# Kernel tuning notes

Hardware: AMD Instinct MI355X
Metric: run time of the kernel (lower is better)

Reference implementation:

```python
import jax, jax.numpy as jnp
import numpy as np
import math

B, D, L, H, K, CONV_N = 32, 128, 1024, 8, 7, 4
DK = D // H
EPS = 1e-5


def make_pos_encoding():
    i = np.arange(D, dtype=np.float64)
    freqs = np.where(i % 2 == 0, 10000.0 ** (-i / D), -(10000.0 ** ((1 - i) / D)))
    phases = np.where(i % 2 == 0, 0.0, math.pi / 2)
    pos = np.arange(L, dtype=np.float64)[None, :]  # [1, L]
    pe = np.sin(pos * freqs[:, None] + phases[:, None])  # [D, L]
    return jnp.asarray(pe, dtype=jnp.float32)


def layer_norm_2d(x, w, b):
    # nn.LayerNorm([D, L]) on [B, D, L]: normalize jointly over last two dims
    mu = jnp.mean(x, axis=(1, 2), keepdims=True)
    var = jnp.var(x, axis=(1, 2), keepdims=True)
    return (x - mu) * jax.lax.rsqrt(var + EPS) * w[None] + b[None]


def setup_inputs():
    key = jax.random.key(0)
    ks = jax.random.split(key, 24)
    s = 0.05
    x = jax.random.normal(ks[0], (B, D, L), jnp.float32)
    lengths = jax.random.randint(ks[1], (B,), L // 2, L + 1)
    mask = (jnp.arange(L)[None, :] >= lengths[:, None]).astype(jnp.float32)  # 1 = pad
    inp = {
        "x": x,
        "mask": mask,
        "pos_enc": make_pos_encoding(),
        "normb_w": jnp.ones((D, L), jnp.float32),
        "normb_b": jnp.zeros((D, L), jnp.float32),
        "dw_w": jax.random.normal(ks[2], (CONV_N, D, K), jnp.float32) * s,
        "dw_b": jnp.zeros((CONV_N, D), jnp.float32),
        "pw_w": jax.random.normal(ks[3], (CONV_N, D, D), jnp.float32) * s,
        "pw_b": jnp.zeros((CONV_N, D), jnp.float32),
        "norms_w": jnp.ones((CONV_N, D, L), jnp.float32),
        "norms_b": jnp.zeros((CONV_N, D, L), jnp.float32),
        "qw": jax.random.normal(ks[4], (D, D), jnp.float32) * s,
        "qb": jnp.zeros((D,), jnp.float32),
        "kw": jax.random.normal(ks[5], (D, D), jnp.float32) * s,
        "kb": jnp.zeros((D,), jnp.float32),
        "vw": jax.random.normal(ks[6], (D, D), jnp.float32) * s,
        "vb": jnp.zeros((D,), jnp.float32),
        "aw": jax.random.normal(ks[7], (D, D), jnp.float32) * s,  # attention output fc
        "ab": jnp.zeros((D,), jnp.float32),
        "norme_w": jnp.ones((D, L), jnp.float32),
        "norme_b": jnp.zeros((D, L), jnp.float32),
        "fw": jax.random.normal(ks[8], (D, D), jnp.float32) * s,  # final fc
        "fb": jnp.zeros((D,), jnp.float32),
    }
    return inp


def reference(x, mask, pos_enc, normb_w, normb_b, dw_w, dw_b, pw_w, pw_b,
              norms_w, norms_b, qw, qb, kw, kb, vw, vb, aw, ab,
              norme_w, norme_b, fw, fb):
    # positional encoding + pre-LN
    out = x + pos_enc[None]
    res = out
    out = layer_norm_2d(out, normb_w, normb_b)

    # conv stack (eval mode: dropout is identity)
    for i in range(CONV_N):
        h = jax.lax.conv_general_dilated(
            out, dw_w[i][:, None, :],  # depthwise: [D, 1, K]
            window_strides=(1,), padding=[(K // 2, K // 2)],
            dimension_numbers=("NCH", "OIH", "NCH"),
            feature_group_count=D) + dw_b[i][None, :, None]
        h = jnp.einsum("bcl,oc->bol", h, pw_w[i]) + pw_b[i][None, :, None]
        out = jax.nn.relu(h) + res
        res = out
        out = layer_norm_2d(out, norms_w[i], norms_b[i])

    # multi-head self-attention (manual bmm-softmax-bmm, scale 1/sqrt(d_k))
    xt = jnp.swapaxes(out, 1, 2)  # [B, L, D]
    q = (xt @ qw.T + qb).reshape(B, L, H, DK)
    k = (xt @ kw.T + kb).reshape(B, L, H, DK)
    v = (xt @ vw.T + vb).reshape(B, L, H, DK)
    scores = jnp.einsum("bqhd,bkhd->bhqk", q, k) * (1.0 / math.sqrt(DK))
    m = mask[:, None, None, :]  # broadcast over heads and query dim
    scores = scores * (1.0 - m) + m * (-1e30)
    attn = jax.nn.softmax(scores, axis=-1)
    o = jnp.einsum("bhqk,bkhd->bqhd", attn, v).reshape(B, L, D)
    o = o @ aw.T + ab
    o = jnp.swapaxes(o, 1, 2)  # [B, D, L]

    out = o + res
    res = out
    out = layer_norm_2d(out, norme_w, norme_b)
    out = jnp.einsum("bdl,ed->bel", out, fw) + fb[None, :, None]
    out = jax.nn.relu(out) + res
    return out
```

## Files before the change

### kernel.cpp

```cpp
#include <hip/hip_runtime.h>

#define NB 32
#define ND 128
#define NL 1024
#define NDL (ND*NL)
#define STATS_B 16
#define STATS_R (32*STATS_B)

typedef __attribute__((ext_vector_type(8))) short bf16x8;
typedef __attribute__((ext_vector_type(4))) float f32x4;

__device__ __forceinline__ f32x4 mfma_bf16_16x16x32(bf16x8 a, bf16x8 b, f32x4 c) {
#if defined(__HIP_DEVICE_COMPILE__)
  return __builtin_amdgcn_mfma_f32_16x16x32_bf16(a, b, c, 0, 0, 0);
#else
  return c;
#endif
}

__device__ __forceinline__ float exp2fast(float x) {
#if defined(__HIP_DEVICE_COMPILE__) && __has_builtin(__builtin_amdgcn_exp2f)
  return __builtin_amdgcn_exp2f(x);
#elif defined(__HIP_DEVICE_COMPILE__)
  return __expf(x * 0.6931471805599453f);
#else
  return x;
#endif
}

__device__ __forceinline__ unsigned short bf16rnd(float f) {
  union { float f; unsigned u; } c; c.f = f;
  return (unsigned short)((c.u + 0x7FFFu + ((c.u >> 16) & 1u)) >> 16);
}
__device__ __forceinline__ unsigned packpair(float a, float b) {
  return (unsigned)bf16rnd(a) | ((unsigned)bf16rnd(b) << 16);
}
__device__ __forceinline__ unsigned packtrunc(float a, float b) {
  unsigned ua = __float_as_uint(a), ub = __float_as_uint(b);
  return (ub & 0xFFFF0000u) | (ua >> 16);
}
__device__ __forceinline__ bf16x8 packbf8(float4 a, float4 b) {
  union { unsigned u[4]; bf16x8 v; } r;
  r.u[0] = packpair(a.x, a.y); r.u[1] = packpair(a.z, a.w);
  r.u[2] = packpair(b.x, b.y); r.u[3] = packpair(b.z, b.w);
  return r.v;
}

__device__ __forceinline__ void blockRedAtomic(float s, float sq, float* base) {
  __shared__ float red[16];
#pragma unroll
  for (int off = 32; off > 0; off >>= 1) {
    s  += __shfl_down(s, off, 64);
    sq += __shfl_down(sq, off, 64);
  }
  int wave = threadIdx.x >> 6;
  int nw = blockDim.x >> 6;
  if ((threadIdx.x & 63) == 0) { red[wave*2] = s; red[wave*2+1] = sq; }
  __syncthreads();
  if (threadIdx.x == 0) {
    float ts = 0.f, tq = 0.f;
    for (int i = 0; i < nw; ++i) { ts += red[i*2]; tq += red[i*2+1]; }
    unsafeAtomicAdd(base,     ts);
    unsafeAtomicAdd(base + 1, tq);
  }
}

__global__ void k_zero(float* stats) {
  int t = threadIdx.x;
#pragma unroll
  for (int i = 0; i < 3; ++i) stats[i*1024 + t] = 0.f;
}

__global__ __launch_bounds__(256) void k_addpos(const float* __restrict__ x,
                                                const float* __restrict__ pe,
                                                float* __restrict__ res,
                                                float* __restrict__ stats0) {
  int b = blockIdx.x >> 6;
  int off = ((blockIdx.x & 63) << 11) + (threadIdx.x << 3);
  const float4* xp = (const float4*)(x + (size_t)b*NDL + off);
  const float4* pp = (const float4*)(pe + off);
  float4* rp = (float4*)(res + (size_t)b*NDL + off);
  float s = 0.f, sq = 0.f;
#pragma unroll
  for (int i = 0; i < 2; ++i) {
    float4 a = xp[i], p = pp[i];
    float4 r;
    r.x = a.x + p.x; r.y = a.y + p.y; r.z = a.z + p.z; r.w = a.w + p.w;
    rp[i] = r;
    s  += r.x + r.y + r.z + r.w;
    sq += r.x*r.x + r.y*r.y + r.z*r.z + r.w*r.w;
  }
  blockRedAtomic(s, sq, stats0 + b*STATS_B);
}


__device__ __forceinline__ void load_w_frags16(const float* __restrict__ W,
                                               int wo, int lo, int hi, bf16x8 af[4]) {
#pragma unroll
  for (int kk = 0; kk < 4; ++kk) {
    const float4* wp = (const float4*)(W + (size_t)(wo + lo)*128 + kk*32 + hi*8);
    af[kk] = packbf8(wp[0], wp[1]);
  }
}

__device__ __forceinline__ void mfma_core16(const unsigned* xs, bf16x8 af[4],
                                            int lo, int hi, f32x4 acc[4]) {
#pragma unroll
  for (int ln = 0; ln < 4; ++ln) {
#pragma unroll
    for (int kk = 0; kk < 4; ++kk) {
      int l = ln*16 + lo;
      int off = (l*256 + kk*64 + hi*16) ^ ((lo & 7) << 4);
      bf16x8 bf = *(const bf16x8*)((const char*)xs + off);
      acc[ln] = mfma_bf16_16x16x32(af[kk], bf, acc[ln]);
    }
  }
}

__device__ __forceinline__ void conv_row(const float* __restrict__ srow,
                                         const float* __restrict__ lwrow,
                                         const float* __restrict__ lbrow,
                                         int base, float mu, float rstd,
                                         const float* wk, float bias0,
                                         float* h ) {
  float wa[14];
  bool interior = (base >= 4) && (base + 12 <= NL);
  if (interior) {
    const float4* sp = (const float4*)(srow + base - 4);
    const float4* wp = (const float4*)(lwrow + base - 4);
    const float4* bp = (const float4*)(lbrow + base - 4);
#pragma unroll
    for (int qd = 0; qd < 4; ++qd) {
      float4 s4 = sp[qd], w4 = wp[qd], b4 = bp[qd];
      float sv[4] = {s4.x, s4.y, s4.z, s4.w};
      float wv[4] = {w4.x, w4.y, w4.z, w4.w};
      float bv[4] = {b4.x, b4.y, b4.z, b4.w};
#pragma unroll
      for (int e = 0; e < 4; ++e) {
        int j = qd*4 + e - 1;
        if (j >= 0 && j < 14)
          wa[j] = (sv[e] - mu)*rstd*wv[e] + bv[e];
      }
    }
  } else {
#pragma unroll
    for (int j = 0; j < 14; ++j) {
      int gl = base + j - 3;
      float v = 0.f;
      if (gl >= 0 && gl < NL)
        v = (srow[gl] - mu)*rstd*lwrow[gl] + lbrow[gl];
      wa[j] = v;
    }
  }
#pragma unroll
  for (int l = 0; l < 8; ++l) {
    float acc = bias0;
#pragma unroll
    for (int j = 0; j < 7; ++j) acc += wa[l+j]*wk[j];
    h[l] = acc;
  }
}

template<int MODE>
__global__ __launch_bounds__(512) void k_gemm_mfma(
    const float* __restrict__ src, const unsigned short* __restrict__ srcb16,
    const float* __restrict__ W, const float* __restrict__ bias,
    const float* __restrict__ resbuf, float* __restrict__ wrbuf,
    const float* __restrict__ lnw, const float* __restrict__ lnb,
    const float* __restrict__ dww, const float* __restrict__ dwb,
    const float* __restrict__ statsIn, float* __restrict__ statsOut) {
  __shared__ unsigned xs[4096];
  int b  = blockIdx.x >> 4;
  int l0 = (blockIdx.x & 15) << 6;
  int tid = threadIdx.x;
  int wave = tid >> 6, lane = tid & 63;
  int lo = lane & 15, hi = lane >> 4;
  int wo = wave * 16;

  float mu = 0.f, rstd = 0.f;
  if (MODE == 0 || MODE == 3) {
    mu = statsIn[b*STATS_B] * (1.f/NDL);
    rstd = rsqrtf(statsIn[b*STATS_B + 1]*(1.f/NDL) - mu*mu + 1e-5f);
  }

  if (MODE == 0) {
    int c2 = tid >> 3, lq = tid & 7;
    int c = c2*2, base = l0 + lq*8;
    float wk0[7], wk1[7];
#pragma unroll
    for (int j = 0; j < 7; ++j) { wk0[j] = dww[c*7 + j]; wk1[j] = dww[(c+1)*7 + j]; }
    const float* sa  = src + (size_t)b*NDL + (size_t)c*NL;
    const float* la  = lnw + (size_t)c*NL;
    const float* lbv = lnb + (size_t)c*NL;
    float h0[8], h1[8];
    conv_row(sa,      la,      lbv,      base, mu, rstd, wk0, dwb[c],   h0);
    conv_row(sa + NL, la + NL, lbv + NL, base, mu, rstd, wk1, dwb[c+1], h1);
#pragma unroll
    for (int l = 0; l < 8; ++l) {
      int ll = lq*8 + l;
      xs[(ll << 6) | (c2 ^ ((ll & 7) << 2))] = packpair(h0[l], h1[l]);
    }
  } else if (MODE == 1) {
    for (int i = tid; i < 1024; i += 512) {
      int c2 = i >> 4, lq = (i & 15) << 2;
      int c = c2*2;
      const unsigned short* sp = srcb16 + (size_t)b*NDL + (size_t)c*NL + l0 + lq;
      uint2 ra = *(const uint2*)sp;
      uint2 rb = *(const uint2*)(sp + NL);
      unsigned wv[4];
      wv[0] = (ra.x & 0xFFFFu) | (rb.x << 16);
      wv[1] = (ra.x >> 16)     | (rb.x & 0xFFFF0000u);
      wv[2] = (ra.y & 0xFFFFu) | (rb.y << 16);
      wv[3] = (ra.y >> 16)     | (rb.y & 0xFFFF0000u);
#pragma unroll
      for (int j = 0; j < 4; ++j) {
        int l = lq + j;
        xs[(l << 6) | (c2 ^ ((l & 7) << 2))] = wv[j];
      }
    }
  } else {
    for (int i = tid; i < 1024; i += 512) {
      int c2 = i >> 4, lq = (i & 15) << 2;
      int c = c2*2;
      const float* sp = src + (size_t)b*NDL + (size_t)c*NL + l0 + lq;
      float4 v0 = *(const float4*)sp;
      float4 v1 = *(const float4*)(sp + NL);
      size_t gi = (size_t)c*NL + l0 + lq;
      float4 w0 = *(const float4*)(lnw + gi), w1 = *(const float4*)(lnw + gi + NL);
      float4 bb0 = *(const float4*)(lnb + gi), bb1 = *(const float4*)(lnb + gi + NL);
      float va[4] = {(v0.x-mu)*rstd*w0.x + bb0.x, (v0.y-mu)*rstd*w0.y + bb0.y,
                     (v0.z-mu)*rstd*w0.z + bb0.z, (v0.w-mu)*rstd*w0.w + bb0.w};
      float vb[4] = {(v1.x-mu)*rstd*w1.x + bb1.x, (v1.y-mu)*rstd*w1.y + bb1.y,
                     (v1.z-mu)*rstd*w1.z + bb1.z, (v1.w-mu)*rstd*w1.w + bb1.w};
#pragma unroll
      for (int j = 0; j < 4; ++j) {
        int l = lq + j;
        xs[(l << 6) | (c2 ^ ((l & 7) << 2))] = packpair(va[j], vb[j]);
      }
    }
  }

  bf16x8 af[4];
  load_w_frags16(W, wo, lo, hi, af);
  f32x4 acc[4];
#pragma unroll
  for (int ln = 0; ln < 4; ++ln) acc[ln] = (f32x4){0.f,0.f,0.f,0.f};

  __syncthreads();
  mfma_core16(xs, af, lo, hi, acc);

  if (MODE == 0 || MODE == 1) {
    float s = 0.f, sq = 0.f;
#pragma unroll
    for (int ln = 0; ln < 4; ++ln) {
      int l = l0 + ln*16 + lo;
#pragma unroll
      for (int r = 0; r < 4; ++r) {
        int o = wo + hi*4 + r;
        size_t gi = ((size_t)b*ND + o)*NL + l;
        float v = acc[ln][r] + bias[o];
        if (MODE == 0) v = fmaxf(v, 0.f);
        v += resbuf[gi];
        wrbuf[gi] = v;
        s += v; sq += v*v;
      }
    }
    blockRedAtomic(s, sq, statsOut + b*STATS_B);
  } else {
#pragma unroll
    for (int ln = 0; ln < 4; ++ln) {
      int l = l0 + ln*16 + lo;
#pragma unroll
      for (int r = 0; r < 4; ++r) {
        int o = wo + hi*4 + r;
        size_t gi = ((size_t)b*ND + o)*NL + l;
        wrbuf[gi] = fmaxf(acc[ln][r] + bias[o], 0.f) + resbuf[gi];
      }
    }
  }
}

__global__ __launch_bounds__(512) void k_qkv_mfma(
    const float* __restrict__ src,
    const float* __restrict__ qw, const float* __restrict__ kw, const float* __restrict__ vw,
    const float* __restrict__ qb, const float* __restrict__ kb, const float* __restrict__ vb,
    unsigned short* __restrict__ qo, unsigned short* __restrict__ ko,
    unsigned short* __restrict__ vo,
    const float* __restrict__ lnw, const float* __restrict__ lnb,
    const float* __restrict__ statsIn) {
  __shared__ unsigned xs[4096];
  int b  = blockIdx.x >> 4;
  int l0 = (blockIdx.x & 15) << 6;
  int tid = threadIdx.x;
  int wave = tid >> 6, lane = tid & 63;
  int lo = lane & 15, hi = lane >> 4;
  int wo = wave * 16;

  float mu = statsIn[b*STATS_B] * (1.f/NDL);
  float rstd = rsqrtf(statsIn[b*STATS_B + 1]*(1.f/NDL) - mu*mu + 1e-5f);
  for (int i = tid; i < 1024; i += 512) {
    int c2 = i >> 4, lq = (i & 15) << 2;
    int c = c2*2;
    const float* sp = src + (size_t)b*NDL + (size_t)c*NL + l0 + lq;
    float4 v0 = *(const float4*)sp;
    float4 v1 = *(const float4*)(sp + NL);
    size_t gi = (size_t)c*NL + l0 + lq;
    float4 w0 = *(const float4*)(lnw + gi), w1 = *(const float4*)(lnw + gi + NL);
    float4 bb0 = *(const float4*)(lnb + gi), bb1 = *(const float4*)(lnb + gi + NL);
    float va[4] = {(v0.x-mu)*rstd*w0.x + bb0.x, (v0.y-mu)*rstd*w0.y + bb0.y,
                   (v0.z-mu)*rstd*w0.z + bb0.z, (v0.w-mu)*rstd*w0.w + bb0.w};
    float vb[4] = {(v1.x-mu)*rstd*w1.x + bb1.x, (v1.y-mu)*rstd*w1.y + bb1.y,
                   (v1.z-mu)*rstd*w1.z + bb1.z, (v1.w-mu)*rstd*w1.w + bb1.w};
#pragma unroll
    for (int j = 0; j < 4; ++j) {
      int l = lq + j;
      xs[(l << 6) | (c2 ^ ((l & 7) << 2))] = packpair(va[j], vb[j]);
    }
  }
  __syncthreads();

  const float* Ws[3] = {qw, kw, vw};
  const float* Bs[3] = {qb, kb, vb};
  unsigned short* Os[3] = {qo, ko, vo};
#pragma unroll 1
  for (int mat = 0; mat < 3; ++mat) {
    bf16x8 af[4];
    load_w_frags16(Ws[mat], wo, lo, hi, af);
    f32x4 acc[4];
#pragma unroll
    for (int ln = 0; ln < 4; ++ln) acc[ln] = (f32x4){0.f,0.f,0.f,0.f};
    mfma_core16(xs, af, lo, hi, acc);
    float oscale = (mat == 0) ? 0.25f*1.4426950408889634f : 1.0f;
    const float* bias = Bs[mat];
    unsigned short* op = Os[mat];
#pragma unroll
    for (int ln = 0; ln < 4; ++ln) {
      int l = l0 + ln*16 + lo;
      int o4 = wo + hi*4;
      float vx = (acc[ln][0] + bias[o4+0]) * oscale;
      float vy = (acc[ln][1] + bias[o4+1]) * oscale;
      float vz = (acc[ln][2] + bias[o4+2]) * oscale;
      float vw4 = (acc[ln][3] + bias[o4+3]) * oscale;
      uint2 pk; pk.x = packpair(vx, vy); pk.y = packpair(vz, vw4);
      *(uint2*)(op + ((size_t)b*NL + l)*ND + o4) = pk;
    }
  }
}

template<bool MASKED>
__device__ __forceinline__ void attn_tile(bf16x8 kf0, bf16x8 kf1, bf16x8 vf,
                                          const bf16x8 qf[4], f32x4 acc[4],
                                          float denp[4], int kb, int len, int hi) {
#pragma unroll
  for (int qt = 0; qt < 4; ++qt) {
    f32x4 z = (f32x4){0.f,0.f,0.f,0.f};
    f32x4 s0 = mfma_bf16_16x16x32(kf0, qf[qt], z);
    f32x4 s1 = mfma_bf16_16x16x32(kf1, qf[qt], z);
    float e[8];
#pragma unroll
    for (int r = 0; r < 4; ++r) {
      float e0 = exp2fast(s0[r]);
      float e1 = exp2fast(s1[r]);
      if (MASKED) {
        e0 = (kb + hi*4 + r < len)      ? e0 : 0.f;
        e1 = (kb + 16 + hi*4 + r < len) ? e1 : 0.f;
      }
      e[r] = e0; e[r+4] = e1;
    }
    denp[qt] += ((e[0]+e[1])+(e[2]+e[3])) + ((e[4]+e[5])+(e[6]+e[7]));
    union { unsigned u[4]; bf16x8 v; } pu;
    pu.u[0] = packtrunc(e[0], e[1]);
    pu.u[1] = packtrunc(e[2], e[3]);
    pu.u[2] = packtrunc(e[4], e[5]);
    pu.u[3] = packtrunc(e[6], e[7]);
    acc[qt] = mfma_bf16_16x16x32(vf, pu.v, acc[qt]);
  }
}

__global__ __launch_bounds__(512) void k_attn_fused(
    const unsigned short* __restrict__ q, const unsigned short* __restrict__ k,
    const unsigned short* __restrict__ v, const float* __restrict__ mask,
    unsigned short* __restrict__ att_t) {
  __shared__ short kv[32768];
  __shared__ int slen_sh;
  int bid = blockIdx.x;
  int b  = bid >> 4;
  int h  = (bid >> 1) & 7;
  int qh = bid & 1;
  int tid = threadIdx.x;
  const float* mrow = mask + (size_t)b*NL;

  if (tid == 0) slen_sh = 0;
  __syncthreads();
  {
    int cnt = 0;
    for (int i = tid; i < NL; i += 512) cnt += (mrow[i] == 0.f) ? 1 : 0;
#pragma unroll
    for (int off = 32; off > 0; off >>= 1) cnt += __shfl_down(cnt, off, 64);
    if ((tid & 63) == 0) atomicAdd(&slen_sh, cnt);
  }
  __syncthreads();
  int len = slen_sh;
  int nkt = (len + 31) >> 5;
  int kstage = nkt << 5;

  for (int idx = tid; idx < 4096; idx += 512) {
    int key = idx >> 2, dq = idx & 3;
    if (key >= kstage) break;
    int dk = dq*4;
    uint2 kd; kd.x = 0u; kd.y = 0u;
    if (key < len) kd = *(const uint2*)(k + ((size_t)b*NL + key)*ND + h*16 + dk);
    int kt = key >> 5, w = key & 31;
    int t16 = w >> 4, klo = w & 15;
    int khi = dk >> 3, ii = dk & 7;
    unsigned* dst = (unsigned*)(kv + kt*512 + t16*256 + (khi*16 + klo)*8 + ii);
    dst[0] = kd.x; dst[1] = kd.y;
  }
  for (int idx = tid; idx < 2048; idx += 512) {
    int keyp = idx >> 2, vq = idx & 3;
    int key = keyp*2;
    if (key >= kstage) break;
    int vlo = vq*4;
    uint2 ra, rb; ra.x = ra.y = rb.x = rb.y = 0u;
    size_t voff = ((size_t)b*NL + key)*ND + h*16 + vlo;
    if (key < len)     ra = *(const uint2*)(v + voff);
    if (key + 1 < len) rb = *(const uint2*)(v + voff + ND);
    unsigned wv[4];
    wv[0] = (ra.x & 0xFFFFu) | (rb.x << 16);
    wv[1] = (ra.x >> 16)     | (rb.x & 0xFFFF0000u);
    wv[2] = (ra.y & 0xFFFFu) | (rb.y << 16);
    wv[3] = (ra.y >> 16)     | (rb.y & 0xFFFF0000u);
    int kt = key >> 5, w = key & 31;
    int vhi, ii;
    if (w < 16) { vhi = w >> 2; ii = w & 3; }
    else        { vhi = (w - 16) >> 2; ii = 4 + (w & 3); }
#pragma unroll
    for (int e = 0; e < 4; ++e)
      *(unsigned*)(kv + 16384 + kt*512 + (vhi*16 + vlo + e)*8 + ii) = wv[e];
  }
  __syncthreads();

  int wave = tid >> 6, lane = tid & 63;
  int lo = lane & 15, hi = lane >> 4;
  int q0 = qh*512 + wave*64;

  bf16x8 qf[4];
#pragma unroll
  for (int qt = 0; qt < 4; ++qt) {
    if (hi < 2) {
      union { uint4 u; bf16x8 v; } qu;
      qu.u = *(const uint4*)(q + ((size_t)b*NL + q0 + qt*16 + lo)*ND + h*16 + hi*8);
      qf[qt] = qu.v;
    } else {
      qf[qt] = (bf16x8){0,0,0,0,0,0,0,0};
    }
  }
  f32x4 acc[4];
  float denp[4];
#pragma unroll
  for (int qt = 0; qt < 4; ++qt) { acc[qt] = (f32x4){0.f,0.f,0.f,0.f}; denp[qt] = 0.f; }

  int fullt = len >> 5;
  int l32 = hi*16 + lo;

  bf16x8 cka = (bf16x8){0,0,0,0,0,0,0,0}, ckb = cka, cv;
  if (hi < 2) {
    cka = *(const bf16x8*)(kv + l32*8);
    ckb = *(const bf16x8*)(kv + 256 + l32*8);
  }
  cv = *(const bf16x8*)(kv + 16384 + lane*8);

  for (int kt = 0; kt < nkt; ++kt) {
    bf16x8 nka = cka, nkb = ckb, nv = cv;
    if (kt + 1 < nkt) {
      if (hi < 2) {
        nka = *(const bf16x8*)(kv + (kt+1)*512 + l32*8);
        nkb = *(const bf16x8*)(kv + (kt+1)*512 + 256 + l32*8);
      }
      nv = *(const bf16x8*)(kv + 16384 + (kt+1)*512 + lane*8);
    }
    if (kt < fullt) attn_tile<false>(cka, ckb, cv, qf, acc, denp, kt*32, len, hi);
    else            attn_tile<true >(cka, ckb, cv, qf, acc, denp, kt*32, len, hi);
    cka = nka; ckb = nkb; cv = nv;
  }
#pragma unroll
  for (int qt = 0; qt < 4; ++qt) {
    float d = denp[qt];
    d += __shfl_xor(d, 16, 64);
    d += __shfl_xor(d, 32, 64);
    float inv = 1.f / d;
    size_t obase = ((size_t)b*ND + h*16)*NL + q0 + qt*16 + lo;
#pragma unroll
    for (int r = 0; r < 4; ++r)
      att_t[obase + (size_t)(hi*4 + r)*NL] = bf16rnd(acc[qt][r] * inv);
  }
}

extern "C" void kernel_launch(void* const* d_in, const int* in_sizes, int n_in,
                              void* d_out, int out_size, void* d_ws, size_t ws_size,
                              hipStream_t stream) {
  (void)in_sizes; (void)n_in; (void)out_size; (void)ws_size;
  const float* x       = (const float*)d_in[0];
  const float* mask    = (const float*)d_in[1];
  const float* pe      = (const float*)d_in[2];
  const float* normb_w = (const float*)d_in[3];
  const float* normb_b = (const float*)d_in[4];
  const float* dw_w    = (const float*)d_in[5];
  const float* dw_b    = (const float*)d_in[6];
  const float* pw_w    = (const float*)d_in[7];
  const float* pw_b    = (const float*)d_in[8];
  const float* norms_w = (const float*)d_in[9];
  const float* norms_b = (const float*)d_in[10];
  const float* qw      = (const float*)d_in[11];
  const float* qb      = (const float*)d_in[12];
  const float* kw      = (const float*)d_in[13];
  const float* kb      = (const float*)d_in[14];
  const float* vw      = (const float*)d_in[15];
  const float* vb      = (const float*)d_in[16];
  const float* aw      = (const float*)d_in[17];
  const float* ab      = (const float*)d_in[18];
  const float* norme_w = (const float*)d_in[19];
  const float* norme_b = (const float*)d_in[20];
  const float* fw      = (const float*)d_in[21];
  const float* fb      = (const float*)d_in[22];

  float* out = (float*)d_out;
  float* ws  = (float*)d_ws;
  const size_t NT = (size_t)NB*ND*NL;
  float* resA = ws;
  float* resB = ws + NT;
  unsigned short* qb16 = (unsigned short*)(ws + 2*NT);
  unsigned short* kb16 = qb16 + NT;
  unsigned short* vb16 = kb16 + NT;
  float* stats = ws + 4*NT;
  unsigned short* att16 = (unsigned short*)resB;

  k_zero<<<dim3(1), dim3(1024), 0, stream>>>(stats);
  k_addpos<<<dim3(2048), dim3(256), 0, stream>>>(x, pe, resA, stats);

  for (int i = 0; i < 4; ++i) {
    const float* lw = (i == 0) ? normb_w : norms_w + (size_t)(i-1)*NDL;
    const float* lb = (i == 0) ? normb_b : norms_b + (size_t)(i-1)*NDL;
    const float* rsrc = (i & 1) ? resB : resA;
    float*       rdst = (i & 1) ? resA : resB;
    k_gemm_mfma<0><<<dim3(NB*16), dim3(512), 0, stream>>>(
        rsrc, nullptr, pw_w + i*ND*ND, pw_b + i*ND, rsrc, rdst,
        lw, lb, dw_w + i*ND*7, dw_b + i*ND,
        stats + i*STATS_R, stats + (i+1)*STATS_R);
  }

  const float* ln3w = norms_w + (size_t)3*NDL;
  const float* ln3b = norms_b + (size_t)3*NDL;
  k_qkv_mfma<<<dim3(NB*16), dim3(512), 0, stream>>>(
      resA, qw, kw, vw, qb, kb, vb, qb16, kb16, vb16, ln3w, ln3b, stats + 4*STATS_R);

  k_attn_fused<<<dim3(NB*8*2), dim3(512), 0, stream>>>(qb16, kb16, vb16, mask, att16);

  k_gemm_mfma<1><<<dim3(NB*16), dim3(512), 0, stream>>>(
      nullptr, att16, aw, ab, resA, resA, nullptr, nullptr, nullptr, nullptr,
      nullptr, stats + 5*STATS_R);
  k_gemm_mfma<3><<<dim3(NB*16), dim3(512), 0, stream>>>(
      resA, nullptr, fw, fb, resA, out, norme_w, norme_b, nullptr, nullptr,
      stats + 5*STATS_R, nullptr);
}
```

Before: 184.3 us.

## Halve GEMM L-tile to 32 columns and compute softmax denominator via MFMA

The pointwise-conv, QKV, attention-output and final-FC GEMM kernels now give each block 32 sequence positions instead of 64. That doubles the grid to 1024 blocks and halves shared memory per block, with the aim of better occupancy and CU coverage on a small problem. The cost is that each block reloads the weight fragments and issues its own stats atomics twice as often. Separately, the attention kernel now gets the softmax denominator from an extra MFMA against a ones vector, replacing the scalar adds and cross-lane shuffles. This computes the sum from bf16-truncated probabilities, which changes numerics slightly.

```diff
diff --git a/kernel.cpp b/kernel.cpp
--- a/kernel.cpp
+++ b/kernel.cpp
@@ -47,7 +47,7 @@
 }
 
 __device__ __forceinline__ void blockRedAtomic(float s, float sq, float* base) {
-  __shared__ float red[16];
+  __shared__ float red[32];
 #pragma unroll
   for (int off = 32; off > 0; off >>= 1) {
     s  += __shfl_down(s, off, 64);
@@ -103,10 +103,10 @@
   }
 }
 
-__device__ __forceinline__ void mfma_core16(const unsigned* xs, bf16x8 af[4],
-                                            int lo, int hi, f32x4 acc[4]) {
-#pragma unroll
-  for (int ln = 0; ln < 4; ++ln) {
+__device__ __forceinline__ void mfma_core32(const unsigned* xs, bf16x8 af[4],
+                                            int lo, int hi, f32x4 acc[2]) {
+#pragma unroll
+  for (int ln = 0; ln < 2; ++ln) {
 #pragma unroll
     for (int kk = 0; kk < 4; ++kk) {
       int l = ln*16 + lo;
@@ -117,20 +117,20 @@
   }
 }
 
-__device__ __forceinline__ void conv_row(const float* __restrict__ srow,
-                                         const float* __restrict__ lwrow,
-                                         const float* __restrict__ lbrow,
-                                         int base, float mu, float rstd,
-                                         const float* wk, float bias0,
-                                         float* h ) {
-  float wa[14];
-  bool interior = (base >= 4) && (base + 12 <= NL);
+__device__ __forceinline__ void conv_row4(const float* __restrict__ srow,
+                                          const float* __restrict__ lwrow,
+                                          const float* __restrict__ lbrow,
+                                          int base, float mu, float rstd,
+                                          const float* wk, float bias0,
+                                          float* h ) {
+  float wa[10];
+  bool interior = (base >= 4) && (base + 8 <= NL);
   if (interior) {
     const float4* sp = (const float4*)(srow + base - 4);
     const float4* wp = (const float4*)(lwrow + base - 4);
     const float4* bp = (const float4*)(lbrow + base - 4);
 #pragma unroll
-    for (int qd = 0; qd < 4; ++qd) {
+    for (int qd = 0; qd < 3; ++qd) {
       float4 s4 = sp[qd], w4 = wp[qd], b4 = bp[qd];
       float sv[4] = {s4.x, s4.y, s4.z, s4.w};
       float wv[4] = {w4.x, w4.y, w4.z, w4.w};
@@ -138,13 +138,13 @@
 #pragma unroll
       for (int e = 0; e < 4; ++e) {
         int j = qd*4 + e - 1;
-        if (j >= 0 && j < 14)
+        if (j >= 0 && j < 10)
           wa[j] = (sv[e] - mu)*rstd*wv[e] + bv[e];
       }
     }
   } else {
 #pragma unroll
-    for (int j = 0; j < 14; ++j) {
+    for (int j = 0; j < 10; ++j) {
       int gl = base + j - 3;
       float v = 0.f;
       if (gl >= 0 && gl < NL)
@@ -153,7 +153,7 @@
     }
   }
 #pragma unroll
-  for (int l = 0; l < 8; ++l) {
+  for (int l = 0; l < 4; ++l) {
     float acc = bias0;
 #pragma unroll
     for (int j = 0; j < 7; ++j) acc += wa[l+j]*wk[j];
@@ -169,9 +169,9 @@
     const float* __restrict__ lnw, const float* __restrict__ lnb,
     const float* __restrict__ dww, const float* __restrict__ dwb,
     const float* __restrict__ statsIn, float* __restrict__ statsOut) {
-  __shared__ unsigned xs[4096];
-  int b  = blockIdx.x >> 4;
-  int l0 = (blockIdx.x & 15) << 6;
+  __shared__ unsigned xs[2048];
+  int b  = blockIdx.x >> 5;
+  int l0 = (blockIdx.x & 31) << 5;
   int tid = threadIdx.x;
   int wave = tid >> 6, lane = tid & 63;
   int lo = lane & 15, hi = lane >> 4;
@@ -183,76 +183,69 @@
     rstd = rsqrtf(statsIn[b*STATS_B + 1]*(1.f/NDL) - mu*mu + 1e-5f);
   }
 
+  int c2 = tid >> 3, lq = (tid & 7) << 2;
+  int c = c2*2;
   if (MODE == 0) {
-    int c2 = tid >> 3, lq = tid & 7;
-    int c = c2*2, base = l0 + lq*8;
+    int base = l0 + lq;
     float wk0[7], wk1[7];
 #pragma unroll
     for (int j = 0; j < 7; ++j) { wk0[j] = dww[c*7 + j]; wk1[j] = dww[(c+1)*7 + j]; }
     const float* sa  = src + (size_t)b*NDL + (size_t)c*NL;
     const float* la  = lnw + (size_t)c*NL;
     const float* lbv = lnb + (size_t)c*NL;
-    float h0[8], h1[8];
-    conv_row(sa,      la,      lbv,      base, mu, rstd, wk0, dwb[c],   h0);
-    conv_row(sa + NL, la + NL, lbv + NL, base, mu, rstd, wk1, dwb[c+1], h1);
-#pragma unroll
-    for (int l = 0; l < 8; ++l) {
-      int ll = lq*8 + l;
+    float h0[4], h1[4];
+    conv_row4(sa,      la,      lbv,      base, mu, rstd, wk0, dwb[c],   h0);
+    conv_row4(sa + NL, la + NL, lbv + NL, base, mu, rstd, wk1, dwb[c+1], h1);
+#pragma unroll
+    for (int l = 0; l < 4; ++l) {
+      int ll = lq + l;
       xs[(ll << 6) | (c2 ^ ((ll & 7) << 2))] = packpair(h0[l], h1[l]);
     }
   } else if (MODE == 1) {
-    for (int i = tid; i < 1024; i += 512) {
-      int c2 = i >> 4, lq = (i & 15) << 2;
-      int c = c2*2;
-      const unsigned short* sp = srcb16 + (size_t)b*NDL + (size_t)c*NL + l0 + lq;
-      uint2 ra = *(const uint2*)sp;
-      uint2 rb = *(const uint2*)(sp + NL);
-      unsigned wv[4];
-      wv[0] = (ra.x & 0xFFFFu) | (rb.x << 16);
-      wv[1] = (ra.x >> 16)     | (rb.x & 0xFFFF0000u);
-      wv[2] = (ra.y & 0xFFFFu) | (rb.y << 16);
-      wv[3] = (ra.y >> 16)     | (rb.y & 0xFFFF0000u);
-#pragma unroll
-      for (int j = 0; j < 4; ++j) {
-        int l = lq + j;
-        xs[(l << 6) | (c2 ^ ((l & 7) << 2))] = wv[j];
-      }
+    const unsigned short* sp = srcb16 + (size_t)b*NDL + (size_t)c*NL + l0 + lq;
+    uint2 ra = *(const uint2*)sp;
+    uint2 rb = *(const uint2*)(sp + NL);
+    unsigned wv[4];
+    wv[0] = (ra.x & 0xFFFFu) | (rb.x << 16);
+    wv[1] = (ra.x >> 16)     | (rb.x & 0xFFFF0000u);
+    wv[2] = (ra.y & 0xFFFFu) | (rb.y << 16);
+    wv[3] = (ra.y >> 16)     | (rb.y & 0xFFFF0000u);
+#pragma unroll
+    for (int j = 0; j < 4; ++j) {
+      int l = lq + j;
+      xs[(l << 6) | (c2 ^ ((l & 7) << 2))] = wv[j];
     }
   } else {
-    for (int i = tid; i < 1024; i += 512) {
-      int c2 = i >> 4, lq = (i & 15) << 2;
-      int c = c2*2;
-      const float* sp = src + (size_t)b*NDL + (size_t)c*NL + l0 + lq;
-      float4 v0 = *(const float4*)sp;
-      float4 v1 = *(const float4*)(sp + NL);
-      size_t gi = (size_t)c*NL + l0 + lq;
-      float4 w0 = *(const float4*)(lnw + gi), w1 = *(const float4*)(lnw + gi + NL);
-      float4 bb0 = *(const float4*)(lnb + gi), bb1 = *(const float4*)(lnb + gi + NL);
-      float va[4] = {(v0.x-mu)*rstd*w0.x + bb0.x, (v0.y-mu)*rstd*w0.y + bb0.y,
-                     (v0.z-mu)*rstd*w0.z + bb0.z, (v0.w-mu)*rstd*w0.w + bb0.w};
-      float vb[4] = {(v1.x-mu)*rstd*w1.x + bb1.x, (v1.y-mu)*rstd*w1.y + bb1.y,
-                     (v1.z-mu)*rstd*w1.z + bb1.z, (v1.w-mu)*rstd*w1.w + bb1.w};
-#pragma unroll
-      for (int j = 0; j < 4; ++j) {
-        int l = lq + j;
-        xs[(l << 6) | (c2 ^ ((l & 7) << 2))] = packpair(va[j], vb[j]);
-      }
+    const float* sp = src + (size_t)b*NDL + (size_t)c*NL + l0 + lq;
+    float4 v0 = *(const float4*)sp;
+    float4 v1 = *(const float4*)(sp + NL);
+    size_t gi = (size_t)c*NL + l0 + lq;
+    float4 w0 = *(const float4*)(lnw + gi), w1 = *(const float4*)(lnw + gi + NL);
+    float4 bb0 = *(const float4*)(lnb + gi), bb1 = *(const float4*)(lnb + gi + NL);
+    float va[4] = {(v0.x-mu)*rstd*w0.x + bb0.x, (v0.y-mu)*rstd*w0.y + bb0.y,
+                   (v0.z-mu)*rstd*w0.z + bb0.z, (v0.w-mu)*rstd*w0.w + bb0.w};
+    float vb[4] = {(v1.x-mu)*rstd*w1.x + bb1.x, (v1.y-mu)*rstd*w1.y + bb1.y,
+                   (v1.z-mu)*rstd*w1.z + bb1.z, (v1.w-mu)*rstd*w1.w + bb1.w};
+#pragma unroll
+    for (int j = 0; j < 4; ++j) {
+      int l = lq + j;
+      xs[(l << 6) | (c2 ^ ((l & 7) << 2))] = packpair(va[j], vb[j]);
     }
   }
 
   bf16x8 af[4];
   load_w_frags16(W, wo, lo, hi, af);
-  f32x4 acc[4];
-#pragma unroll
-  for (int ln = 0; ln < 4; ++ln) acc[ln] = (f32x4){0.f,0.f,0.f,0.f};
+  f32x4 acc[2];
+#pragma unroll
+  for (int ln = 0; ln < 2; ++ln) acc[ln] = (f32x4){0.f,0.f,0.f,0.f};
 
   __syncthreads();
-  mfma_core16(xs, af, lo, hi, acc);
+  mfma_core32(xs, af, lo, hi, acc);
 
   if (MODE == 0 || MODE == 1) {
     float s = 0.f, sq = 0.f;
 #pragma unroll
-    for (int ln = 0; ln < 4; ++ln) {
+    for (int ln = 0; ln < 2; ++ln) {
       int l = l0 + ln*16 + lo;
 #pragma unroll
       for (int r = 0; r < 4; ++r) {
@@ -268,7 +261,7 @@
     blockRedAtomic(s, sq, statsOut + b*STATS_B);
   } else {
 #pragma unroll
-    for (int ln = 0; ln < 4; ++ln) {
+    for (int ln = 0; ln < 2; ++ln) {
       int l = l0 + ln*16 + lo;
 #pragma unroll
       for (int r = 0; r < 4; ++r) {
@@ -288,9 +281,9 @@
     unsigned short* __restrict__ vo,
     const float* __restrict__ lnw, const float* __restrict__ lnb,
     const float* __restrict__ statsIn) {
-  __shared__ unsigned xs[4096];
-  int b  = blockIdx.x >> 4;
-  int l0 = (blockIdx.x & 15) << 6;
+  __shared__ unsigned xs[2048];
+  int b  = blockIdx.x >> 5;
+  int l0 = (blockIdx.x & 31) << 5;
   int tid = threadIdx.x;
   int wave = tid >> 6, lane = tid & 63;
   int lo = lane & 15, hi = lane >> 4;
@@ -298,8 +291,8 @@
 
   float mu = statsIn[b*STATS_B] * (1.f/NDL);
   float rstd = rsqrtf(statsIn[b*STATS_B + 1]*(1.f/NDL) - mu*mu + 1e-5f);
-  for (int i = tid; i < 1024; i += 512) {
-    int c2 = i >> 4, lq = (i & 15) << 2;
+  {
+    int c2 = tid >> 3, lq = (tid & 7) << 2;
     int c = c2*2;
     const float* sp = src + (size_t)b*NDL + (size_t)c*NL + l0 + lq;
     float4 v0 = *(const float4*)sp;
@@ -326,15 +319,15 @@
   for (int mat = 0; mat < 3; ++mat) {
     bf16x8 af[4];
     load_w_frags16(Ws[mat], wo, lo, hi, af);
-    f32x4 acc[4];
-#pragma unroll
-    for (int ln = 0; ln < 4; ++ln) acc[ln] = (f32x4){0.f,0.f,0.f,0.f};
-    mfma_core16(xs, af, lo, hi, acc);
+    f32x4 acc[2];
+#pragma unroll
+    for (int ln = 0; ln < 2; ++ln) acc[ln] = (f32x4){0.f,0.f,0.f,0.f};
+    mfma_core32(xs, af, lo, hi, acc);
     float oscale = (mat == 0) ? 0.25f*1.4426950408889634f : 1.0f;
     const float* bias = Bs[mat];
     unsigned short* op = Os[mat];
 #pragma unroll
-    for (int ln = 0; ln < 4; ++ln) {
+    for (int ln = 0; ln < 2; ++ln) {
       int l = l0 + ln*16 + lo;
       int o4 = wo + hi*4;
       float vx = (acc[ln][0] + bias[o4+0]) * oscale;
@@ -349,8 +342,9 @@
 
 template<bool MASKED>
 __device__ __forceinline__ void attn_tile(bf16x8 kf0, bf16x8 kf1, bf16x8 vf,
-                                          const bf16x8 qf[4], f32x4 acc[4],
-                                          float denp[4], int kb, int len, int hi) {
+                                          bf16x8 onesf, const bf16x8 qf[4],
+                                          f32x4 acc[4], f32x4 dacc[4],
+                                          int kb, int len, int hi) {
 #pragma unroll
   for (int qt = 0; qt < 4; ++qt) {
     f32x4 z = (f32x4){0.f,0.f,0.f,0.f};
@@ -367,13 +361,13 @@
       }
       e[r] = e0; e[r+4] = e1;
     }
-    denp[qt] += ((e[0]+e[1])+(e[2]+e[3])) + ((e[4]+e[5])+(e[6]+e[7]));
     union { unsigned u[4]; bf16x8 v; } pu;
     pu.u[0] = packtrunc(e[0], e[1]);
     pu.u[1] = packtrunc(e[2], e[3]);
     pu.u[2] = packtrunc(e[4], e[5]);
     pu.u[3] = packtrunc(e[6], e[7]);
-    acc[qt] = mfma_bf16_16x16x32(vf, pu.v, acc[qt]);
+    acc[qt]  = mfma_bf16_16x16x32(vf,    pu.v, acc[qt]);
+    dacc[qt] = mfma_bf16_16x16x32(onesf, pu.v, dacc[qt]);
   }
 }
 
@@ -455,10 +449,14 @@
       qf[qt] = (bf16x8){0,0,0,0,0,0,0,0};
     }
   }
-  f32x4 acc[4];
-  float denp[4];
-#pragma unroll
-  for (int qt = 0; qt < 4; ++qt) { acc[qt] = (f32x4){0.f,0.f,0.f,0.f}; denp[qt] = 0.f; }
+  const short oneb = (short)0x3F80;
+  bf16x8 onesf = (bf16x8){oneb,oneb,oneb,oneb,oneb,oneb,oneb,oneb};
+  f32x4 acc[4], dacc[4];
+#pragma unroll
+  for (int qt = 0; qt < 4; ++qt) {
+    acc[qt]  = (f32x4){0.f,0.f,0.f,0.f};
+    dacc[qt] = (f32x4){0.f,0.f,0.f,0.f};
+  }
 
   int fullt = len >> 5;
   int l32 = hi*16 + lo;
@@ -479,16 +477,13 @@
       }
       nv = *(const bf16x8*)(kv + 16384 + (kt+1)*512 + lane*8);
     }
-    if (kt < fullt) attn_tile<false>(cka, ckb, cv, qf, acc, denp, kt*32, len, hi);
-    else            attn_tile<true >(cka, ckb, cv, qf, acc, denp, kt*32, len, hi);
+    if (kt < fullt) attn_tile<false>(cka, ckb, cv, onesf, qf, acc, dacc, kt*32, len, hi);
+    else            attn_tile<true >(cka, ckb, cv, onesf, qf, acc, dacc, kt*32, len, hi);
     cka = nka; ckb = nkb; cv = nv;
   }
 #pragma unroll
   for (int qt = 0; qt < 4; ++qt) {
-    float d = denp[qt];
-    d += __shfl_xor(d, 16, 64);
-    d += __shfl_xor(d, 32, 64);
-    float inv = 1.f / d;
+    float inv = 1.f / dacc[qt][0];
     size_t obase = ((size_t)b*ND + h*16)*NL + q0 + qt*16 + lo;
 #pragma unroll
     for (int r = 0; r < 4; ++r)
@@ -543,7 +538,7 @@
     const float* lb = (i == 0) ? normb_b : norms_b + (size_t)(i-1)*NDL;
     const float* rsrc = (i & 1) ? resB : resA;
     float*       rdst = (i & 1) ? resA : resB;
-    k_gemm_mfma<0><<<dim3(NB*16), dim3(512), 0, stream>>>(
+    k_gemm_mfma<0><<<dim3(NB*32), dim3(512), 0, stream>>>(
         rsrc, nullptr, pw_w + i*ND*ND, pw_b + i*ND, rsrc, rdst,
         lw, lb, dw_w + i*ND*7, dw_b + i*ND,
         stats + i*STATS_R, stats + (i+1)*STATS_R);
@@ -551,15 +546,15 @@
 
   const float* ln3w = norms_w + (size_t)3*NDL;
   const float* ln3b = norms_b + (size_t)3*NDL;
-  k_qkv_mfma<<<dim3(NB*16), dim3(512), 0, stream>>>(
+  k_qkv_mfma<<<dim3(NB*32), dim3(512), 0, stream>>>(
       resA, qw, kw, vw, qb, kb, vb, qb16, kb16, vb16, ln3w, ln3b, stats + 4*STATS_R);
 
   k_attn_fused<<<dim3(NB*8*2), dim3(512), 0, stream>>>(qb16, kb16, vb16, mask, att16);
 
-  k_gemm_mfma<1><<<dim3(NB*16), dim3(512), 0, stream>>>(
+  k_gemm_mfma<1><<<dim3(NB*32), dim3(512), 0, stream>>>(
       nullptr, att16, aw, ab, resA, resA, nullptr, nullptr, nullptr, nullptr,
       nullptr, stats + 5*STATS_R);
-  k_gemm_mfma<3><<<dim3(NB*16), dim3(512), 0, stream>>>(
+  k_gemm_mfma<3><<<dim3(NB*32), dim3(512), 0, stream>>>(
       resA, nullptr, fw, fb, resA, out, norme_w, norme_b, nullptr, nullptr,
       stats + 5*STATS_R, nullptr);
 }
```

Measured after the change: 224.3 us. 21.7% more time.

## Store residual stream in bf16 and compute softmax denominator via MFMA

Applied to the files above, without the earlier changes.

The fp32 residual buffers that pass between the add-pos, conv-GEMM, QKV and output kernels now hold bf16, and each consumer widens values back to fp32 on load. This halves global memory traffic for reading and writing the residual in every stage. Separately, the attention kernel computes the softmax row sum with an extra MFMA against a ones vector instead of scalar adds and cross-lane shuffles. Accumulating the residual in bf16 across the conv layers adds rounding error at each step, and the denominator now sums the truncated bf16 probabilities rather than the fp32 ones.

```diff
diff --git a/kernel.cpp b/kernel.cpp
--- a/kernel.cpp
+++ b/kernel.cpp
@@ -9,6 +9,7 @@
 
 typedef __attribute__((ext_vector_type(8))) short bf16x8;
 typedef __attribute__((ext_vector_type(4))) float f32x4;
+typedef unsigned short u16;
 
 __device__ __forceinline__ f32x4 mfma_bf16_16x16x32(bf16x8 a, bf16x8 b, f32x4 c) {
 #if defined(__HIP_DEVICE_COMPILE__)
@@ -28,9 +29,12 @@
 #endif
 }
 
-__device__ __forceinline__ unsigned short bf16rnd(float f) {
+__device__ __forceinline__ float bf2f(u16 u) {
+  union { unsigned u; float f; } c; c.u = ((unsigned)u) << 16; return c.f;
+}
+__device__ __forceinline__ u16 bf16rnd(float f) {
   union { float f; unsigned u; } c; c.f = f;
-  return (unsigned short)((c.u + 0x7FFFu + ((c.u >> 16) & 1u)) >> 16);
+  return (u16)((c.u + 0x7FFFu + ((c.u >> 16) & 1u)) >> 16);
 }
 __device__ __forceinline__ unsigned packpair(float a, float b) {
   return (unsigned)bf16rnd(a) | ((unsigned)bf16rnd(b) << 16);
@@ -47,7 +51,7 @@
 }
 
 __device__ __forceinline__ void blockRedAtomic(float s, float sq, float* base) {
-  __shared__ float red[16];
+  __shared__ float red[32];
 #pragma unroll
   for (int off = 32; off > 0; off >>= 1) {
     s  += __shfl_down(s, off, 64);
@@ -73,23 +77,26 @@
 
 __global__ __launch_bounds__(256) void k_addpos(const float* __restrict__ x,
                                                 const float* __restrict__ pe,
-                                                float* __restrict__ res,
+                                                u16* __restrict__ res,
                                                 float* __restrict__ stats0) {
   int b = blockIdx.x >> 6;
   int off = ((blockIdx.x & 63) << 11) + (threadIdx.x << 3);
   const float4* xp = (const float4*)(x + (size_t)b*NDL + off);
   const float4* pp = (const float4*)(pe + off);
-  float4* rp = (float4*)(res + (size_t)b*NDL + off);
   float s = 0.f, sq = 0.f;
+  float rv[8];
 #pragma unroll
   for (int i = 0; i < 2; ++i) {
     float4 a = xp[i], p = pp[i];
-    float4 r;
-    r.x = a.x + p.x; r.y = a.y + p.y; r.z = a.z + p.z; r.w = a.w + p.w;
-    rp[i] = r;
-    s  += r.x + r.y + r.z + r.w;
-    sq += r.x*r.x + r.y*r.y + r.z*r.z + r.w*r.w;
-  }
+    rv[i*4+0] = a.x + p.x; rv[i*4+1] = a.y + p.y;
+    rv[i*4+2] = a.z + p.z; rv[i*4+3] = a.w + p.w;
+  }
+#pragma unroll
+  for (int j = 0; j < 8; ++j) { s += rv[j]; sq += rv[j]*rv[j]; }
+  uint4 pk;
+  pk.x = packpair(rv[0], rv[1]); pk.y = packpair(rv[2], rv[3]);
+  pk.z = packpair(rv[4], rv[5]); pk.w = packpair(rv[6], rv[7]);
+  *(uint4*)(res + (size_t)b*NDL + off) = pk;
   blockRedAtomic(s, sq, stats0 + b*STATS_B);
 }
 
@@ -117,22 +124,24 @@
   }
 }
 
-__device__ __forceinline__ void conv_row(const float* __restrict__ srow,
-                                         const float* __restrict__ lwrow,
-                                         const float* __restrict__ lbrow,
-                                         int base, float mu, float rstd,
-                                         const float* wk, float bias0,
-                                         float* h ) {
+__device__ __forceinline__ void conv_row8(const u16* __restrict__ srow,
+                                          const float* __restrict__ lwrow,
+                                          const float* __restrict__ lbrow,
+                                          int base, float mu, float rstd,
+                                          const float* wk, float bias0,
+                                          float* h ) {
   float wa[14];
   bool interior = (base >= 4) && (base + 12 <= NL);
   if (interior) {
-    const float4* sp = (const float4*)(srow + base - 4);
+    const uint2* sp = (const uint2*)(srow + base - 4);
     const float4* wp = (const float4*)(lwrow + base - 4);
     const float4* bp = (const float4*)(lbrow + base - 4);
 #pragma unroll
     for (int qd = 0; qd < 4; ++qd) {
-      float4 s4 = sp[qd], w4 = wp[qd], b4 = bp[qd];
-      float sv[4] = {s4.x, s4.y, s4.z, s4.w};
+      uint2 sv2 = sp[qd];
+      float4 w4 = wp[qd], b4 = bp[qd];
+      float sv[4] = {bf2f((u16)(sv2.x & 0xFFFF)), bf2f((u16)(sv2.x >> 16)),
+                     bf2f((u16)(sv2.y & 0xFFFF)), bf2f((u16)(sv2.y >> 16))};
       float wv[4] = {w4.x, w4.y, w4.z, w4.w};
       float bv[4] = {b4.x, b4.y, b4.z, b4.w};
 #pragma unroll
@@ -148,7 +157,7 @@
       int gl = base + j - 3;
       float v = 0.f;
       if (gl >= 0 && gl < NL)
-        v = (srow[gl] - mu)*rstd*lwrow[gl] + lbrow[gl];
+        v = (bf2f(srow[gl]) - mu)*rstd*lwrow[gl] + lbrow[gl];
       wa[j] = v;
     }
   }
@@ -163,9 +172,10 @@
 
 template<int MODE>
 __global__ __launch_bounds__(512) void k_gemm_mfma(
-    const float* __restrict__ src, const unsigned short* __restrict__ srcb16,
-    const float* __restrict__ W, const float* __restrict__ bias,
-    const float* __restrict__ resbuf, float* __restrict__ wrbuf,
+    const u16* __restrict__ src16, const float* __restrict__ W,
+    const float* __restrict__ bias,
+    const u16* __restrict__ res16, u16* __restrict__ wr16,
+    float* __restrict__ outf,
     const float* __restrict__ lnw, const float* __restrict__ lnb,
     const float* __restrict__ dww, const float* __restrict__ dwb,
     const float* __restrict__ statsIn, float* __restrict__ statsOut) {
@@ -189,12 +199,12 @@
     float wk0[7], wk1[7];
 #pragma unroll
     for (int j = 0; j < 7; ++j) { wk0[j] = dww[c*7 + j]; wk1[j] = dww[(c+1)*7 + j]; }
-    const float* sa  = src + (size_t)b*NDL + (size_t)c*NL;
+    const u16* sa = src16 + (size_t)b*NDL + (size_t)c*NL;
     const float* la  = lnw + (size_t)c*NL;
     const float* lbv = lnb + (size_t)c*NL;
     float h0[8], h1[8];
-    conv_row(sa,      la,      lbv,      base, mu, rstd, wk0, dwb[c],   h0);
-    conv_row(sa + NL, la + NL, lbv + NL, base, mu, rstd, wk1, dwb[c+1], h1);
+    conv_row8(sa,      la,      lbv,      base, mu, rstd, wk0, dwb[c],   h0);
+    conv_row8(sa + NL, la + NL, lbv + NL, base, mu, rstd, wk1, dwb[c+1], h1);
 #pragma unroll
     for (int l = 0; l < 8; ++l) {
       int ll = lq*8 + l;
@@ -204,7 +214,7 @@
     for (int i = tid; i < 1024; i += 512) {
       int c2 = i >> 4, lq = (i & 15) << 2;
       int c = c2*2;
-      const unsigned short* sp = srcb16 + (size_t)b*NDL + (size_t)c*NL + l0 + lq;
+      const u16* sp = src16 + (size_t)b*NDL + (size_t)c*NL + l0 + lq;
       uint2 ra = *(const uint2*)sp;
       uint2 rb = *(const uint2*)(sp + NL);
       unsigned wv[4];
@@ -222,16 +232,20 @@
     for (int i = tid; i < 1024; i += 512) {
       int c2 = i >> 4, lq = (i & 15) << 2;
       int c = c2*2;
-      const float* sp = src + (size_t)b*NDL + (size_t)c*NL + l0 + lq;
-      float4 v0 = *(const float4*)sp;
-      float4 v1 = *(const float4*)(sp + NL);
+      const u16* sp = src16 + (size_t)b*NDL + (size_t)c*NL + l0 + lq;
+      uint2 ra = *(const uint2*)sp;
+      uint2 rb = *(const uint2*)(sp + NL);
+      float sa[4] = {bf2f((u16)(ra.x & 0xFFFF)), bf2f((u16)(ra.x >> 16)),
+                     bf2f((u16)(ra.y & 0xFFFF)), bf2f((u16)(ra.y >> 16))};
+      float sb[4] = {bf2f((u16)(rb.x & 0xFFFF)), bf2f((u16)(rb.x >> 16)),
+                     bf2f((u16)(rb.y & 0xFFFF)), bf2f((u16)(rb.y >> 16))};
       size_t gi = (size_t)c*NL + l0 + lq;
       float4 w0 = *(const float4*)(lnw + gi), w1 = *(const float4*)(lnw + gi + NL);
       float4 bb0 = *(const float4*)(lnb + gi), bb1 = *(const float4*)(lnb + gi + NL);
-      float va[4] = {(v0.x-mu)*rstd*w0.x + bb0.x, (v0.y-mu)*rstd*w0.y + bb0.y,
-                     (v0.z-mu)*rstd*w0.z + bb0.z, (v0.w-mu)*rstd*w0.w + bb0.w};
-      float vb[4] = {(v1.x-mu)*rstd*w1.x + bb1.x, (v1.y-mu)*rstd*w1.y + bb1.y,
-                     (v1.z-mu)*rstd*w1.z + bb1.z, (v1.w-mu)*rstd*w1.w + bb1.w};
+      float va[4] = {(sa[0]-mu)*rstd*w0.x + bb0.x, (sa[1]-mu)*rstd*w0.y + bb0.y,
+                     (sa[2]-mu)*rstd*w0.z + bb0.z, (sa[3]-mu)*rstd*w0.w + bb0.w};
+      float vb[4] = {(sb[0]-mu)*rstd*w1.x + bb1.x, (sb[1]-mu)*rstd*w1.y + bb1.y,
+                     (sb[2]-mu)*rstd*w1.z + bb1.z, (sb[3]-mu)*rstd*w1.w + bb1.w};
 #pragma unroll
       for (int j = 0; j < 4; ++j) {
         int l = lq + j;
@@ -260,8 +274,8 @@
         size_t gi = ((size_t)b*ND + o)*NL + l;
         float v = acc[ln][r] + bias[o];
         if (MODE == 0) v = fmaxf(v, 0.f);
-        v += resbuf[gi];
-        wrbuf[gi] = v;
+        v += bf2f(res16[gi]);
+        wr16[gi] = bf16rnd(v);
         s += v; sq += v*v;
       }
     }
@@ -274,18 +288,17 @@
       for (int r = 0; r < 4; ++r) {
         int o = wo + hi*4 + r;
         size_t gi = ((size_t)b*ND + o)*NL + l;
-        wrbuf[gi] = fmaxf(acc[ln][r] + bias[o], 0.f) + resbuf[gi];
+        outf[gi] = fmaxf(acc[ln][r] + bias[o], 0.f) + bf2f(res16[gi]);
       }
     }
   }
 }
 
 __global__ __launch_bounds__(512) void k_qkv_mfma(
-    const float* __restrict__ src,
+    const u16* __restrict__ src16,
     const float* __restrict__ qw, const float* __restrict__ kw, const float* __restrict__ vw,
     const float* __restrict__ qb, const float* __restrict__ kb, const float* __restrict__ vb,
-    unsigned short* __restrict__ qo, unsigned short* __restrict__ ko,
-    unsigned short* __restrict__ vo,
+    u16* __restrict__ qo, u16* __restrict__ ko, u16* __restrict__ vo,
     const float* __restrict__ lnw, const float* __restrict__ lnb,
     const float* __restrict__ statsIn) {
   __shared__ unsigned xs[4096];
@@ -301,27 +314,31 @@
   for (int i = tid; i < 1024; i += 512) {
     int c2 = i >> 4, lq = (i & 15) << 2;
     int c = c2*2;
-    const float* sp = src + (size_t)b*NDL + (size_t)c*NL + l0 + lq;
-    float4 v0 = *(const float4*)sp;
-    float4 v1 = *(const float4*)(sp + NL);
+    const u16* sp = src16 + (size_t)b*NDL + (size_t)c*NL + l0 + lq;
+    uint2 ra = *(const uint2*)sp;
+    uint2 rb = *(const uint2*)(sp + NL);
+    float sa[4] = {bf2f((u16)(ra.x & 0xFFFF)), bf2f((u16)(ra.x >> 16)),
+                   bf2f((u16)(ra.y & 0xFFFF)), bf2f((u16)(ra.y >> 16))};
+    float sb[4] = {bf2f((u16)(rb.x & 0xFFFF)), bf2f((u16)(rb.x >> 16)),
+                   bf2f((u16)(rb.y & 0xFFFF)), bf2f((u16)(rb.y >> 16))};
     size_t gi = (size_t)c*NL + l0 + lq;
     float4 w0 = *(const float4*)(lnw + gi), w1 = *(const float4*)(lnw + gi + NL);
     float4 bb0 = *(const float4*)(lnb + gi), bb1 = *(const float4*)(lnb + gi + NL);
-    float va[4] = {(v0.x-mu)*rstd*w0.x + bb0.x, (v0.y-mu)*rstd*w0.y + bb0.y,
-                   (v0.z-mu)*rstd*w0.z + bb0.z, (v0.w-mu)*rstd*w0.w + bb0.w};
-    float vb[4] = {(v1.x-mu)*rstd*w1.x + bb1.x, (v1.y-mu)*rstd*w1.y + bb1.y,
-                   (v1.z-mu)*rstd*w1.z + bb1.z, (v1.w-mu)*rstd*w1.w + bb1.w};
+    float va[4] = {(sa[0]-mu)*rstd*w0.x + bb0.x, (sa[1]-mu)*rstd*w0.y + bb0.y,
+                   (sa[2]-mu)*rstd*w0.z + bb0.z, (sa[3]-mu)*rstd*w0.w + bb0.w};
+    float vb4[4] = {(sb[0]-mu)*rstd*w1.x + bb1.x, (sb[1]-mu)*rstd*w1.y + bb1.y,
+                    (sb[2]-mu)*rstd*w1.z + bb1.z, (sb[3]-mu)*rstd*w1.w + bb1.w};
 #pragma unroll
     for (int j = 0; j < 4; ++j) {
       int l = lq + j;
-      xs[(l << 6) | (c2 ^ ((l & 7) << 2))] = packpair(va[j], vb[j]);
+      xs[(l << 6) | (c2 ^ ((l & 7) << 2))] = packpair(va[j], vb4[j]);
     }
   }
   __syncthreads();
 
   const float* Ws[3] = {qw, kw, vw};
   const float* Bs[3] = {qb, kb, vb};
-  unsigned short* Os[3] = {qo, ko, vo};
+  u16* Os[3] = {qo, ko, vo};
 #pragma unroll 1
   for (int mat = 0; mat < 3; ++mat) {
     bf16x8 af[4];
@@ -332,7 +349,7 @@
     mfma_core16(xs, af, lo, hi, acc);
     float oscale = (mat == 0) ? 0.25f*1.4426950408889634f : 1.0f;
     const float* bias = Bs[mat];
-    unsigned short* op = Os[mat];
+    u16* op = Os[mat];
 #pragma unroll
     for (int ln = 0; ln < 4; ++ln) {
       int l = l0 + ln*16 + lo;
@@ -349,8 +366,9 @@
 
 template<bool MASKED>
 __device__ __forceinline__ void attn_tile(bf16x8 kf0, bf16x8 kf1, bf16x8 vf,
-                                          const bf16x8 qf[4], f32x4 acc[4],
-                                          float denp[4], int kb, int len, int hi) {
+                                          bf16x8 onesf, const bf16x8 qf[4],
+                                          f32x4 acc[4], f32x4 dacc[4],
+                                          int kb, int len, int hi) {
 #pragma unroll
   for (int qt = 0; qt < 4; ++qt) {
     f32x4 z = (f32x4){0.f,0.f,0.f,0.f};
@@ -367,20 +385,20 @@
       }
       e[r] = e0; e[r+4] = e1;
     }
-    denp[qt] += ((e[0]+e[1])+(e[2]+e[3])) + ((e[4]+e[5])+(e[6]+e[7]));
     union { unsigned u[4]; bf16x8 v; } pu;
     pu.u[0] = packtrunc(e[0], e[1]);
     pu.u[1] = packtrunc(e[2], e[3]);
     pu.u[2] = packtrunc(e[4], e[5]);
     pu.u[3] = packtrunc(e[6], e[7]);
-    acc[qt] = mfma_bf16_16x16x32(vf, pu.v, acc[qt]);
+    acc[qt]  = mfma_bf16_16x16x32(vf,    pu.v, acc[qt]);
+    dacc[qt] = mfma_bf16_16x16x32(onesf, pu.v, dacc[qt]);
   }
 }
 
 __global__ __launch_bounds__(512) void k_attn_fused(
-    const unsigned short* __restrict__ q, const unsigned short* __restrict__ k,
-    const unsigned short* __restrict__ v, const float* __restrict__ mask,
-    unsigned short* __restrict__ att_t) {
+    const u16* __restrict__ q, const u16* __restrict__ k,
+    const u16* __restrict__ v, const float* __restrict__ mask,
+    u16* __restrict__ att_t) {
   __shared__ short kv[32768];
   __shared__ int slen_sh;
   int bid = blockIdx.x;
@@ -455,10 +473,14 @@
       qf[qt] = (bf16x8){0,0,0,0,0,0,0,0};
     }
   }
-  f32x4 acc[4];
-  float denp[4];
-#pragma unroll
-  for (int qt = 0; qt < 4; ++qt) { acc[qt] = (f32x4){0.f,0.f,0.f,0.f}; denp[qt] = 0.f; }
+  const short oneb = (short)0x3F80;
+  bf16x8 onesf = (bf16x8){oneb,oneb,oneb,oneb,oneb,oneb,oneb,oneb};
+  f32x4 acc[4], dacc[4];
+#pragma unroll
+  for (int qt = 0; qt < 4; ++qt) {
+    acc[qt]  = (f32x4){0.f,0.f,0.f,0.f};
+    dacc[qt] = (f32x4){0.f,0.f,0.f,0.f};
+  }
 
   int fullt = len >> 5;
   int l32 = hi*16 + lo;
@@ -479,16 +501,13 @@
       }
       nv = *(const bf16x8*)(kv + 16384 + (kt+1)*512 + lane*8);
     }
-    if (kt < fullt) attn_tile<false>(cka, ckb, cv, qf, acc, denp, kt*32, len, hi);
-    else            attn_tile<true >(cka, ckb, cv, qf, acc, denp, kt*32, len, hi);
+    if (kt < fullt) attn_tile<false>(cka, ckb, cv, onesf, qf, acc, dacc, kt*32, len, hi);
+    else            attn_tile<true >(cka, ckb, cv, onesf, qf, acc, dacc, kt*32, len, hi);
     cka = nka; ckb = nkb; cv = nv;
   }
 #pragma unroll
   for (int qt = 0; qt < 4; ++qt) {
-    float d = denp[qt];
-    d += __shfl_xor(d, 16, 64);
-    d += __shfl_xor(d, 32, 64);
-    float inv = 1.f / d;
+    float inv = 1.f / dacc[qt][0];
     size_t obase = ((size_t)b*ND + h*16)*NL + q0 + qt*16 + lo;
 #pragma unroll
     for (int r = 0; r < 4; ++r)
@@ -527,13 +546,13 @@
   float* out = (float*)d_out;
   float* ws  = (float*)d_ws;
   const size_t NT = (size_t)NB*ND*NL;
-  float* resA = ws;
-  float* resB = ws + NT;
-  unsigned short* qb16 = (unsigned short*)(ws + 2*NT);
-  unsigned short* kb16 = qb16 + NT;
-  unsigned short* vb16 = kb16 + NT;
-  float* stats = ws + 4*NT;
-  unsigned short* att16 = (unsigned short*)resB;
+  u16* resA = (u16*)ws;
+  u16* resB = (u16*)(ws + NT/2);
+  u16* qb16 = (u16*)(ws + NT);
+  u16* kb16 = (u16*)(ws + 3*NT/2);
+  u16* vb16 = (u16*)(ws + 2*NT);
+  float* stats = ws + 3*NT;
+  u16* att16 = resB;
 
   k_zero<<<dim3(1), dim3(1024), 0, stream>>>(stats);
   k_addpos<<<dim3(2048), dim3(256), 0, stream>>>(x, pe, resA, stats);
@@ -541,10 +560,10 @@
   for (int i = 0; i < 4; ++i) {
     const float* lw = (i == 0) ? normb_w : norms_w + (size_t)(i-1)*NDL;
     const float* lb = (i == 0) ? normb_b : norms_b + (size_t)(i-1)*NDL;
-    const float* rsrc = (i & 1) ? resB : resA;
-    float*       rdst = (i & 1) ? resA : resB;
+    const u16* rsrc = (i & 1) ? resB : resA;
+    u16*       rdst = (i & 1) ? resA : resB;
     k_gemm_mfma<0><<<dim3(NB*16), dim3(512), 0, stream>>>(
-        rsrc, nullptr, pw_w + i*ND*ND, pw_b + i*ND, rsrc, rdst,
+        rsrc, pw_w + i*ND*ND, pw_b + i*ND, rsrc, rdst, nullptr,
         lw, lb, dw_w + i*ND*7, dw_b + i*ND,
         stats + i*STATS_R, stats + (i+1)*STATS_R);
   }
@@ -557,9 +576,9 @@
   k_attn_fused<<<dim3(NB*8*2), dim3(512), 0, stream>>>(qb16, kb16, vb16, mask, att16);
 
   k_gemm_mfma<1><<<dim3(NB*16), dim3(512), 0, stream>>>(
-      nullptr, att16, aw, ab, resA, resA, nullptr, nullptr, nullptr, nullptr,
+      att16, aw, ab, resA, resA, nullptr, nullptr, nullptr, nullptr, nullptr,
       nullptr, stats + 5*STATS_R);
   k_gemm_mfma<3><<<dim3(NB*16), dim3(512), 0, stream>>>(
-      resA, nullptr, fw, fb, resA, out, norme_w, norme_b, nullptr, nullptr,
+      resA, fw, fb, resA, nullptr, out, norme_w, norme_b, nullptr, nullptr,
       stats + 5*STATS_R, nullptr);
 }
```

Measured after the change: 173.0 us. -6.1%, faster.
